# Optimization experiments

Hardware: AMD Instinct MI355X
Metric: run time of the kernel (lower is better)

The kernel has to match this reference:

```python
import jax, jax.numpy as jnp
import numpy as np

STRIDE = 1
PADDING = 1


def setup_inputs() -> dict:
    key = jax.random.key(0)
    kx, kw = jax.random.split(key)
    B, Cin, H, W = 32, 64, 112, 112
    Cout, K = 64, 3
    x = jax.random.normal(kx, (B, Cin, H, W), dtype=jnp.float32)
    # ternary latent weights in {-1, 0, 1}, stored as float (matches torch.randint(-1,2).float())
    w = jax.random.randint(kw, (Cout, Cin, K, K), -1, 2).astype(jnp.float32)
    bias = jnp.zeros((Cout,), dtype=jnp.float32)
    scale = jnp.float32(1.0)
    return {"x": x, "w": w, "bias": bias, "scale": scale}


def reference(x, w, bias, scale):
    # Straight-through sign quantization: forward uses sign(w), grad passes to w.
    w_q = w + jax.lax.stop_gradient(jnp.sign(w) - w)
    # conv2d, NCHW / OIHW layout, stride 1, pad 1
    y = jax.lax.conv_general_dilated(
        x, w_q,
        window_strides=(STRIDE, STRIDE),
        padding=[(PADDING, PADDING), (PADDING, PADDING)],
        dimension_numbers=("NCHW", "OIHW", "NCHW"),
    )
    # fused bias + scale: out = scale * (conv + bias)
    # (grad_bias in the original backward is sum(grad_out * scale), implying bias is inside the scale)
    return scale * (y + bias[None, :, None, None])
```

## Files before the change

kernel.cpp:

```cpp
#include <hip/hip_runtime.h>

#define B_ 32
#define C_ 64
#define H_ 112
#define W_ 112
#define HW (H_ * W_)
#define HTILES 56
#define NBLKC (B_ * HTILES)

#define SLOTS 114
#define CHUNK 128
#define XROWB (SLOTS * CHUNK)
#define XT_BYTES ((size_t)B_ * H_ * XROWB)
#define WQ_OFF 131072

typedef short bf16x8 __attribute__((ext_vector_type(8)));
typedef float f32x4 __attribute__((ext_vector_type(4)));
typedef unsigned int u32;

#define GLOAD_LDS(g, l, sz)                                                   \
    __builtin_amdgcn_global_load_lds(                                         \
        (const __attribute__((address_space(1))) u32*)(const void*)(g),       \
        (__attribute__((address_space(3))) u32*)(void*)(l), (sz), 0, 0)

__device__ inline unsigned short f2bf(float f) {
    union { float f; unsigned u; } v;
    v.f = f;
    unsigned u = v.u;
    u += 0x7fffu + ((u >> 16) & 1u);
    return (unsigned short)(u >> 16);
}

__global__ __launch_bounds__(256) void xform(const float* __restrict__ x,
                                             unsigned short* __restrict__ xt,
                                             const float* __restrict__ w,
                                             unsigned short* __restrict__ wq2) {
    __shared__ unsigned short pl[C_ * SLOTS];

    const int tid = threadIdx.x;
    const int b   = blockIdx.x / H_;
    const int h   = blockIdx.x % H_;

#pragma unroll
    for (int it = 0; it < 7; ++it) {
        const int u  = tid + 256 * it;
        const int c  = u / 28;
        const int w4 = u % 28;
        const f32x4 v =
            *(const f32x4*)(x + ((size_t)(b * C_ + c) * H_ + h) * W_ + w4 * 4);
        const u32 lo = (u32)f2bf(v[0]) | ((u32)f2bf(v[1]) << 16);
        const u32 hi = (u32)f2bf(v[2]) | ((u32)f2bf(v[3]) << 16);
        u32* p = (u32*)&pl[c * SLOTS + w4 * 4];
        p[0] = lo;
        p[1] = hi;
    }
    __syncthreads();

    unsigned short* xtrow = xt + (size_t)(b * H_ + h) * (XROWB / 2);
#pragma unroll
    for (int it = 0; it < 15; ++it) {
        const int u = tid + 256 * it;
        if (u < SLOTS * 32) {
            const int slot = u >> 5;
            const int cp   = u & 31;
            u32 val = 0;
            if (1 <= slot && slot <= 112) {
                const int ww = slot - 1;
                val = (u32)pl[(2 * cp) * SLOTS + ww] |
                      ((u32)pl[(2 * cp + 1) * SLOTS + ww] << 16);
            }
            *(u32*)((char*)xtrow + slot * CHUNK +
                    ((cp * 4) ^ ((slot & 7) << 4))) = val;
        }
    }

    if (blockIdx.x < 18) {
        const int i = blockIdx.x * 256 + tid;
        const int lane = i & 63;
        const int t    = (i >> 6) % 36;
        const int mw   = i / 2304;
        const int shift = t >> 2;
        const int c0    = (t >> 1) & 1;
        const int m     = t & 1;
        const int dh = shift / 3, dw = shift % 3;
        const int lcol = lane & 15, kg = lane >> 4;
        const int cout = mw * 32 + m * 16 + lcol;
        const int cinb = c0 * 32 + kg * 8;
        unsigned short pk[8];
#pragma unroll
        for (int j = 0; j < 8; ++j) {
            const float v = w[((cout * C_ + cinb + j) * 3 + dh) * 3 + dw];
            pk[j] = (v > 0.f) ? (unsigned short)0x3F80
                              : ((v < 0.f) ? (unsigned short)0xBF80
                                           : (unsigned short)0);
        }
        bf16x8 pv;
#pragma unroll
        for (int j = 0; j < 8; ++j) pv[j] = (short)pk[j];
        *(bf16x8*)((char*)wq2 + ((size_t)(mw * 36 + t) * 64 + lane) * 16) = pv;
    }
}

__global__ __launch_bounds__(256, 2) void conv_mfma(
    const unsigned short* __restrict__ xt, const unsigned short* __restrict__ wq2,
    const float* __restrict__ bias, const float* __restrict__ scale,
    float* __restrict__ out) {
    __shared__ char xs[4 * XROWB];

    const int tid  = threadIdx.x;
    const int lane = tid & 63;
    const int wave = tid >> 6;
    const int lcol = lane & 15;
    const int kg   = lane >> 4;
    const int mw   = wave >> 1;
    const int nw   = wave & 1;

    const int bid = blockIdx.x;
    const int s   = (bid & 7) * (NBLKC / 8) + (bid >> 3);
    const int b   = s / HTILES;
    const int h0  = (s % HTILES) * 2;

    const char* xtc = (const char*)xt + (size_t)b * H_ * XROWB;

    bf16x8 wt[36];
    {
        const char* wp = (const char*)wq2 + (size_t)mw * 36 * 1024 + lane * 16;
#pragma unroll
        for (int t = 0; t < 36; ++t) wt[t] = *(const bf16x8*)(wp + t * 1024);
    }

    {
        const int r    = wave;
        const int xrow = h0 - 1 + r;
        char* dst = xs + r * XROWB;
        if (0 <= xrow && xrow < H_) {
            const char* src = xtc + (size_t)xrow * XROWB + lane * 16;
#pragma unroll
            for (int ch = 0; ch < 14; ++ch)
                GLOAD_LDS(src + ch * 1024, dst + ch * 1024, 16);
            GLOAD_LDS(xtc + (size_t)xrow * XROWB + 14336 + lane * 4,
                      dst + 14336, 4);
        } else {
            char* d = dst + lane * 16;
            const f32x4 z = {0.f, 0.f, 0.f, 0.f};
#pragma unroll
            for (int ch = 0; ch < 14; ++ch) *(f32x4*)(d + ch * 1024) = z;
            *(u32*)(dst + 14336 + lane * 4) = 0u;
        }
    }
    __syncthreads();

    int koff[3][2];
#pragma unroll
    for (int dw = 0; dw < 3; ++dw) {
        const int key = ((lcol + dw) & 7) << 4;
        koff[dw][0] = (kg * 16) ^ key;
        koff[dw][1] = (64 + kg * 16) ^ key;
    }

    f32x4 acc[2][7];
#pragma unroll
    for (int m = 0; m < 2; ++m)
#pragma unroll
        for (int nf = 0; nf < 7; ++nf) acc[m][nf] = (f32x4){0.f, 0.f, 0.f, 0.f};

#pragma unroll
    for (int dh = 0; dh < 3; ++dh) {
        const char* rowb = xs + (nw + dh) * XROWB;
#pragma unroll
        for (int dw = 0; dw < 3; ++dw) {
            const char* colb = rowb + (lcol + dw) * CHUNK;
#pragma unroll
            for (int c0 = 0; c0 < 2; ++c0) {
                const int t0 = ((dh * 3 + dw) * 2 + c0) * 2;
                const char* cb = colb + koff[dw][c0];
#pragma unroll
                for (int nf = 0; nf < 7; ++nf) {
                    const bf16x8 bv = *(const bf16x8*)(cb + nf * 2048);
                    acc[0][nf] = __builtin_amdgcn_mfma_f32_16x16x32_bf16(
                        wt[t0 + 0], bv, acc[0][nf], 0, 0, 0);
                    acc[1][nf] = __builtin_amdgcn_mfma_f32_16x16x32_bf16(
                        wt[t0 + 1], bv, acc[1][nf], 0, 0, 0);
                }
            }
        }
    }

    const float sc = scale[0];
    const int h = h0 + nw;
#pragma unroll
    for (int m = 0; m < 2; ++m) {
        const int cobase = mw * 32 + m * 16 + kg * 4;
        const f32x4 bs = *(const f32x4*)(bias + cobase);
#pragma unroll
        for (int nf = 0; nf < 7; ++nf) {
            const int col = nf * 16 + lcol;
#pragma unroll
            for (int rr = 0; rr < 4; ++rr)
                out[((size_t)(b * C_ + cobase + rr)) * HW + h * W_ + col] =
                    sc * (acc[m][nf][rr] + bs[rr]);
        }
    }
}

extern "C" void kernel_launch(void* const* d_in, const int* in_sizes, int n_in,
                              void* d_out, int out_size, void* d_ws,
                              size_t ws_size, hipStream_t stream) {
    const float* x     = (const float*)d_in[0];
    const float* w     = (const float*)d_in[1];
    const float* bias  = (const float*)d_in[2];
    const float* scale = (const float*)d_in[3];
    float* out         = (float*)d_out;

    unsigned short* wq2 = (unsigned short*)d_ws;
    unsigned short* xt  = (unsigned short*)((char*)d_ws + WQ_OFF);

    xform<<<B_ * H_, 256, 0, stream>>>(x, xt, w, wq2);
    conv_mfma<<<NBLKC, 256, 0, stream>>>(xt, wq2, bias, scale, out);
}
```

Before: 64.64 us.

## Split conv row staging into two LDS halves to overlap load with compute

The conv kernel now stages each input row in two column halves (slots 0-65 and 64-113). The second half's async global-to-LDS loads are issued after the first barrier, so they overlap the MFMA compute and stores for output columns 0-63. A second barrier precedes compute on columns 64-111. This hides part of the load latency and cuts accumulator registers per phase, but it adds a barrier and a small redundant overlap of staged slots.

```diff
diff --git a/kernel.cpp b/kernel.cpp
--- a/kernel.cpp
+++ b/kernel.cpp
@@ -13,6 +13,12 @@
 #define XROWB (SLOTS * CHUNK)
 #define XT_BYTES ((size_t)B_ * H_ * XROWB)
 #define WQ_OFF 131072
+
+#define AROWB (66 * CHUNK)
+#define ABUFB (4 * AROWB)
+#define BROWB (50 * CHUNK)
+#define BBUFB (4 * BROWB)
+#define XS_B (ABUFB + BBUFB)
 
 typedef short bf16x8 __attribute__((ext_vector_type(8)));
 typedef float f32x4 __attribute__((ext_vector_type(4)));
@@ -75,7 +81,7 @@
     }
 
     if (blockIdx.x < 18) {
-        const int i = blockIdx.x * 256 + tid;
+        const int i    = blockIdx.x * 256 + tid;
         const int lane = i & 63;
         const int t    = (i >> 6) % 36;
         const int mw   = i / 2304;
@@ -86,17 +92,14 @@
         const int lcol = lane & 15, kg = lane >> 4;
         const int cout = mw * 32 + m * 16 + lcol;
         const int cinb = c0 * 32 + kg * 8;
-        unsigned short pk[8];
+        bf16x8 pv;
 #pragma unroll
         for (int j = 0; j < 8; ++j) {
             const float v = w[((cout * C_ + cinb + j) * 3 + dh) * 3 + dw];
-            pk[j] = (v > 0.f) ? (unsigned short)0x3F80
-                              : ((v < 0.f) ? (unsigned short)0xBF80
-                                           : (unsigned short)0);
-        }
-        bf16x8 pv;
-#pragma unroll
-        for (int j = 0; j < 8; ++j) pv[j] = (short)pk[j];
+            pv[j] = (v > 0.f) ? (short)0x3F80
+                              : ((v < 0.f) ? (short)(unsigned short)0xBF80
+                                           : (short)0);
+        }
         *(bf16x8*)((char*)wq2 + ((size_t)(mw * 36 + t) * 64 + lane) * 16) = pv;
     }
 }
@@ -105,7 +108,7 @@
     const unsigned short* __restrict__ xt, const unsigned short* __restrict__ wq2,
     const float* __restrict__ bias, const float* __restrict__ scale,
     float* __restrict__ out) {
-    __shared__ char xs[4 * XROWB];
+    __shared__ char xs[XS_B];
 
     const int tid  = threadIdx.x;
     const int lane = tid & 63;
@@ -121,6 +124,8 @@
     const int h0  = (s % HTILES) * 2;
 
     const char* xtc = (const char*)xt + (size_t)b * H_ * XROWB;
+    char* bufA = xs;
+    char* bufB = xs + ABUFB;
 
     bf16x8 wt[36];
     {
@@ -129,26 +134,38 @@
         for (int t = 0; t < 36; ++t) wt[t] = *(const bf16x8*)(wp + t * 1024);
     }
 
-    {
-        const int r    = wave;
-        const int xrow = h0 - 1 + r;
-        char* dst = xs + r * XROWB;
-        if (0 <= xrow && xrow < H_) {
-            const char* src = xtc + (size_t)xrow * XROWB + lane * 16;
-#pragma unroll
-            for (int ch = 0; ch < 14; ++ch)
-                GLOAD_LDS(src + ch * 1024, dst + ch * 1024, 16);
-            GLOAD_LDS(xtc + (size_t)xrow * XROWB + 14336 + lane * 4,
-                      dst + 14336, 4);
-        } else {
-            char* d = dst + lane * 16;
-            const f32x4 z = {0.f, 0.f, 0.f, 0.f};
-#pragma unroll
-            for (int ch = 0; ch < 14; ++ch) *(f32x4*)(d + ch * 1024) = z;
-            *(u32*)(dst + 14336 + lane * 4) = 0u;
-        }
+    const int xrow = h0 - 1 + wave;
+    const bool inb = (0 <= xrow) && (xrow < H_);
+    const char* srow = xtc + (size_t)xrow * XROWB;
+    char* dA = bufA + wave * AROWB;
+    char* dB = bufB + wave * BROWB;
+
+    if (inb) {
+        const char* srcA = srow + lane * 16;
+#pragma unroll
+        for (int ch = 0; ch < 8; ++ch)
+            GLOAD_LDS(srcA + ch * 1024, dA + ch * 1024, 16);
+        GLOAD_LDS(srow + 8192 + lane * 4, dA + 8192, 4);
+    } else {
+        const f32x4 z = {0.f, 0.f, 0.f, 0.f};
+#pragma unroll
+        for (int ch = 0; ch < 8; ++ch)
+            *(f32x4*)(dA + lane * 16 + ch * 1024) = z;
+        if (lane < 16) *(f32x4*)(dA + 8192 + lane * 16) = z;
+#pragma unroll
+        for (int ch = 0; ch < 6; ++ch)
+            *(f32x4*)(dB + lane * 16 + ch * 1024) = z;
+        if (lane < 16) *(f32x4*)(dB + 6144 + lane * 16) = z;
     }
     __syncthreads();
+
+    if (inb) {
+        const char* srcB = srow + 8192 + lane * 16;
+#pragma unroll
+        for (int ch = 0; ch < 6; ++ch)
+            GLOAD_LDS(srcB + ch * 1024, dB + ch * 1024, 16);
+        GLOAD_LDS(srow + 14336 + lane * 4, dB + 6144, 4);
+    }
 
     int koff[3][2];
 #pragma unroll
@@ -158,47 +175,101 @@
         koff[dw][1] = (64 + kg * 16) ^ key;
     }
 
-    f32x4 acc[2][7];
+    const float sc = scale[0];
+    f32x4 bs[2];
 #pragma unroll
     for (int m = 0; m < 2; ++m)
-#pragma unroll
-        for (int nf = 0; nf < 7; ++nf) acc[m][nf] = (f32x4){0.f, 0.f, 0.f, 0.f};
-
-#pragma unroll
-    for (int dh = 0; dh < 3; ++dh) {
-        const char* rowb = xs + (nw + dh) * XROWB;
-#pragma unroll
-        for (int dw = 0; dw < 3; ++dw) {
-            const char* colb = rowb + (lcol + dw) * CHUNK;
-#pragma unroll
-            for (int c0 = 0; c0 < 2; ++c0) {
-                const int t0 = ((dh * 3 + dw) * 2 + c0) * 2;
-                const char* cb = colb + koff[dw][c0];
-#pragma unroll
-                for (int nf = 0; nf < 7; ++nf) {
-                    const bf16x8 bv = *(const bf16x8*)(cb + nf * 2048);
-                    acc[0][nf] = __builtin_amdgcn_mfma_f32_16x16x32_bf16(
-                        wt[t0 + 0], bv, acc[0][nf], 0, 0, 0);
-                    acc[1][nf] = __builtin_amdgcn_mfma_f32_16x16x32_bf16(
-                        wt[t0 + 1], bv, acc[1][nf], 0, 0, 0);
+        bs[m] = *(const f32x4*)(bias + mw * 32 + m * 16 + kg * 4);
+
+    {
+        f32x4 acc[2][4];
+#pragma unroll
+        for (int m = 0; m < 2; ++m)
+#pragma unroll
+            for (int nf = 0; nf < 4; ++nf)
+                acc[m][nf] = (f32x4){0.f, 0.f, 0.f, 0.f};
+
+#pragma unroll
+        for (int dh = 0; dh < 3; ++dh) {
+            const char* rowb = bufA + (nw + dh) * AROWB;
+#pragma unroll
+            for (int dw = 0; dw < 3; ++dw) {
+                const char* colb = rowb + (lcol + dw) * CHUNK;
+#pragma unroll
+                for (int c0 = 0; c0 < 2; ++c0) {
+                    const int t0 = ((dh * 3 + dw) * 2 + c0) * 2;
+                    const char* cb = colb + koff[dw][c0];
+#pragma unroll
+                    for (int nf = 0; nf < 4; ++nf) {
+                        const bf16x8 bv = *(const bf16x8*)(cb + nf * 2048);
+                        acc[0][nf] = __builtin_amdgcn_mfma_f32_16x16x32_bf16(
+                            wt[t0 + 0], bv, acc[0][nf], 0, 0, 0);
+                        acc[1][nf] = __builtin_amdgcn_mfma_f32_16x16x32_bf16(
+                            wt[t0 + 1], bv, acc[1][nf], 0, 0, 0);
+                    }
                 }
             }
         }
-    }
-
-    const float sc = scale[0];
-    const int h = h0 + nw;
-#pragma unroll
-    for (int m = 0; m < 2; ++m) {
-        const int cobase = mw * 32 + m * 16 + kg * 4;
-        const f32x4 bs = *(const f32x4*)(bias + cobase);
-#pragma unroll
-        for (int nf = 0; nf < 7; ++nf) {
-            const int col = nf * 16 + lcol;
-#pragma unroll
-            for (int rr = 0; rr < 4; ++rr)
-                out[((size_t)(b * C_ + cobase + rr)) * HW + h * W_ + col] =
-                    sc * (acc[m][nf][rr] + bs[rr]);
+
+        const int h = h0 + nw;
+#pragma unroll
+        for (int m = 0; m < 2; ++m) {
+            const int cobase = mw * 32 + m * 16 + kg * 4;
+#pragma unroll
+            for (int nf = 0; nf < 4; ++nf) {
+                const int col = nf * 16 + lcol;
+#pragma unroll
+                for (int rr = 0; rr < 4; ++rr)
+                    out[((size_t)(b * C_ + cobase + rr)) * HW + h * W_ + col] =
+                        sc * (acc[m][nf][rr] + bs[m][rr]);
+            }
+        }
+    }
+
+    __syncthreads();
+
+    {
+        f32x4 acc[2][3];
+#pragma unroll
+        for (int m = 0; m < 2; ++m)
+#pragma unroll
+            for (int nf = 0; nf < 3; ++nf)
+                acc[m][nf] = (f32x4){0.f, 0.f, 0.f, 0.f};
+
+#pragma unroll
+        for (int dh = 0; dh < 3; ++dh) {
+            const char* rowb = bufB + (nw + dh) * BROWB;
+#pragma unroll
+            for (int dw = 0; dw < 3; ++dw) {
+                const char* colb = rowb + (lcol + dw) * CHUNK;
+#pragma unroll
+                for (int c0 = 0; c0 < 2; ++c0) {
+                    const int t0 = ((dh * 3 + dw) * 2 + c0) * 2;
+                    const char* cb = colb + koff[dw][c0];
+#pragma unroll
+                    for (int nf = 0; nf < 3; ++nf) {
+                        const bf16x8 bv = *(const bf16x8*)(cb + nf * 2048);
+                        acc[0][nf] = __builtin_amdgcn_mfma_f32_16x16x32_bf16(
+                            wt[t0 + 0], bv, acc[0][nf], 0, 0, 0);
+                        acc[1][nf] = __builtin_amdgcn_mfma_f32_16x16x32_bf16(
+                            wt[t0 + 1], bv, acc[1][nf], 0, 0, 0);
+                    }
+                }
+            }
+        }
+
+        const int h = h0 + nw;
+#pragma unroll
+        for (int m = 0; m < 2; ++m) {
+            const int cobase = mw * 32 + m * 16 + kg * 4;
+#pragma unroll
+            for (int nf = 0; nf < 3; ++nf) {
+                const int col = 64 + nf * 16 + lcol;
+#pragma unroll
+                for (int rr = 0; rr < 4; ++rr)
+                    out[((size_t)(b * C_ + cobase + rr)) * HW + h * W_ + col] =
+                        sc * (acc[m][nf][rr] + bs[m][rr]);
+            }
         }
     }
 }
```

Measured after the change: 65.79 us. Within noise of the previous version (+1.8%).
